# Kernel tuning notes

Measured on AMD Instinct MI355X. Metric: run time of the kernel, lower is better.

## Reference

```python
import jax, jax.numpy as jnp
import numpy as np

# Intersection(mode='product'):
#   a_fk = a @ feats.T            # [Na, K]
#   b_fk = b @ feats.T            # [Nb, K]
#   mask = (a_fk[:,None,:] > 0) & (b_fk[None,:,:] > 0)
#   result = sum_k (a_fk[:,None,:] * b_fk[None,:,:]) * mask   # [Na, Nb]
# For the product op, (x*y)*[x>0 & y>0] == relu(x)*relu(y) elementwise
# (any term with a non-positive factor is zeroed either way), so the
# broadcast+mask+reduce collapses exactly into a GEMM over relu'd scores.

def setup_inputs() -> dict:
    key = jax.random.key(0)
    k1, k2, k3 = jax.random.split(key, 3)
    a = jax.random.normal(k1, (1024, 2048), dtype=jnp.float32)
    b = jax.random.normal(k2, (1024, 2048), dtype=jnp.float32)
    feats = jax.random.normal(k3, (128, 2048), dtype=jnp.float32)
    return {"a": a, "b": b, "feats": feats}

def reference(a, b, feats):
    a_fk = a @ feats.T            # [Na, K]
    b_fk = b @ feats.T            # [Nb, K]
    # masked product-intersection reduced over K; identical math to the
    # broadcast (Na, Nb, K) -> sum formulation of the torch module.
    return jnp.einsum('ak,bk->ab', jax.nn.relu(a_fk), jax.nn.relu(b_fk))
```

## Files before the change

kernel.cpp:

```cpp
#include <hip/hip_runtime.h>


typedef __attribute__((ext_vector_type(8))) __bf16 bf16x8;
typedef __attribute__((ext_vector_type(4))) __bf16 bf16x4;
typedef __attribute__((ext_vector_type(4))) float floatx4;

#define KD     2048
#define NF     128
#define NA     1024
#define NPART  16
#define FKN    (2048 * 128)

static __device__ inline bf16x8 cvt8(float4 u, float4 v) {
    bf16x8 s;
    s[0] = (__bf16)u.x; s[1] = (__bf16)u.y; s[2] = (__bf16)u.z; s[3] = (__bf16)u.w;
    s[4] = (__bf16)v.x; s[5] = (__bf16)v.y; s[6] = (__bf16)v.z; s[7] = (__bf16)v.w;
    return s;
}

__global__ __launch_bounds__(256) void gemm1_part(const float* __restrict__ A,
                                                  const float* __restrict__ B,
                                                  const float* __restrict__ F,
                                                  float* __restrict__ part) {
    __shared__ __bf16 Xs[64 * 40];
    __shared__ __bf16 Fs[128 * 40];

    const int t    = threadIdx.x;
    const int m0   = blockIdx.x * 64;
    const int s    = blockIdx.y;
    const int k0   = s * 128;
    const float* src = (m0 < NA) ? (A + (size_t)m0 * KD)
                                 : (B + (size_t)(m0 - NA) * KD);

    const int lane = t & 63;
    const int w    = t >> 6;
    const int ln   = lane & 15;
    const int quad = lane >> 4;
    const int q8   = quad * 8;

    floatx4 acc[4][2];
#pragma unroll
    for (int mt = 0; mt < 4; mt++)
#pragma unroll
        for (int nt = 0; nt < 2; nt++)
            acc[mt][nt] = (floatx4){0.f, 0.f, 0.f, 0.f};

    const int xrow = t >> 2, xcol = (t & 3) * 8;
    const int frow = t >> 1, fcol = (t & 1) * 16;

#pragma unroll
    for (int kk = 0; kk < 128; kk += 32) {
        {
            const float* p = src + (size_t)xrow * KD + (k0 + kk + xcol);
            float4 u = *(const float4*)p;
            float4 v = *(const float4*)(p + 4);
            *(bf16x8*)&Xs[xrow * 40 + xcol] = cvt8(u, v);
        }
        {
            const float* p = F + (size_t)frow * KD + (k0 + kk + fcol);
            float4 u0 = *(const float4*)(p + 0);
            float4 u1 = *(const float4*)(p + 4);
            float4 u2 = *(const float4*)(p + 8);
            float4 u3 = *(const float4*)(p + 12);
            *(bf16x8*)&Fs[frow * 40 + fcol]     = cvt8(u0, u1);
            *(bf16x8*)&Fs[frow * 40 + fcol + 8] = cvt8(u2, u3);
        }
        __syncthreads();

        bf16x8 bfrag[2];
#pragma unroll
        for (int nt = 0; nt < 2; nt++)
            bfrag[nt] = *(const bf16x8*)&Fs[(w * 32 + nt * 16 + ln) * 40 + q8];
#pragma unroll
        for (int mt = 0; mt < 4; mt++) {
            bf16x8 af = *(const bf16x8*)&Xs[(mt * 16 + ln) * 40 + q8];
#pragma unroll
            for (int nt = 0; nt < 2; nt++)
                acc[mt][nt] = __builtin_amdgcn_mfma_f32_16x16x32_bf16(
                    af, bfrag[nt], acc[mt][nt], 0, 0, 0);
        }
        __syncthreads();
    }

    float* pdst = part + (size_t)s * FKN;
#pragma unroll
    for (int mt = 0; mt < 4; mt++)
#pragma unroll
        for (int nt = 0; nt < 2; nt++)
#pragma unroll
            for (int r = 0; r < 4; r++) {
                int row = m0 + mt * 16 + quad * 4 + r;
                int col = w * 32 + nt * 16 + ln;
                pdst[(size_t)row * NF + col] = acc[mt][nt][r];
            }
}

__global__ __launch_bounds__(256) void reduce_relu(const float* __restrict__ part,
                                                   __bf16* __restrict__ fkb) {
    int idx = blockIdx.x * 256 + threadIdx.x;
    size_t base = (size_t)idx * 4;
    float4 sum = make_float4(0.f, 0.f, 0.f, 0.f);
#pragma unroll
    for (int s = 0; s < NPART; s++) {
        float4 u = *(const float4*)(part + (size_t)s * FKN + base);
        sum.x += u.x; sum.y += u.y; sum.z += u.z; sum.w += u.w;
    }
    bf16x4 o;
    o[0] = (__bf16)fmaxf(sum.x, 0.f);
    o[1] = (__bf16)fmaxf(sum.y, 0.f);
    o[2] = (__bf16)fmaxf(sum.z, 0.f);
    o[3] = (__bf16)fmaxf(sum.w, 0.f);
    *(bf16x4*)(fkb + base) = o;
}

__global__ __launch_bounds__(256) void gemm2(const __bf16* __restrict__ fkb,
                                             float* __restrict__ out) {
    __shared__ __bf16 Ps[64 * 136];
    __shared__ __bf16 Qs[64 * 136];

    const int t    = threadIdx.x;
    const int i0   = blockIdx.y * 64;
    const int j0   = blockIdx.x * 64;
    const int lane = t & 63;
    const int w    = t >> 6;
    const int wm   = w & 1;
    const int wn   = w >> 1;
    const int ln   = lane & 15;
    const int quad = lane >> 4;
    const int q8   = quad * 8;

    const int prow = t >> 2, pcol = (t & 3) * 32;
    {
        const __bf16* p = fkb + (size_t)(i0 + prow) * NF + pcol;
        const __bf16* q = fkb + (size_t)(NA + j0 + prow) * NF + pcol;
#pragma unroll
        for (int c = 0; c < 32; c += 8) {
            *(bf16x8*)&Ps[prow * 136 + pcol + c] = *(const bf16x8*)(p + c);
            *(bf16x8*)&Qs[prow * 136 + pcol + c] = *(const bf16x8*)(q + c);
        }
    }
    __syncthreads();

    floatx4 acc[2][2];
#pragma unroll
    for (int mt = 0; mt < 2; mt++)
#pragma unroll
        for (int nt = 0; nt < 2; nt++)
            acc[mt][nt] = (floatx4){0.f, 0.f, 0.f, 0.f};

#pragma unroll
    for (int k0 = 0; k0 < 128; k0 += 32) {
        bf16x8 af[2], bf[2];
#pragma unroll
        for (int mt = 0; mt < 2; mt++)
            af[mt] = *(const bf16x8*)&Ps[(wm * 32 + mt * 16 + ln) * 136 + k0 + q8];
#pragma unroll
        for (int nt = 0; nt < 2; nt++)
            bf[nt] = *(const bf16x8*)&Qs[(wn * 32 + nt * 16 + ln) * 136 + k0 + q8];
#pragma unroll
        for (int mt = 0; mt < 2; mt++)
#pragma unroll
            for (int nt = 0; nt < 2; nt++)
                acc[mt][nt] = __builtin_amdgcn_mfma_f32_16x16x32_bf16(
                    af[mt], bf[nt], acc[mt][nt], 0, 0, 0);
    }

#pragma unroll
    for (int mt = 0; mt < 2; mt++)
#pragma unroll
        for (int nt = 0; nt < 2; nt++)
#pragma unroll
            for (int r = 0; r < 4; r++) {
                int row = i0 + wm * 32 + mt * 16 + quad * 4 + r;
                int col = j0 + wn * 32 + nt * 16 + ln;
                out[(size_t)row * 1024 + col] = acc[mt][nt][r];
            }
}

extern "C" void kernel_launch(void* const* d_in, const int* in_sizes, int n_in,
                              void* d_out, int out_size, void* d_ws, size_t ws_size,
                              hipStream_t stream) {
    const float* a     = (const float*)d_in[0];
    const float* b     = (const float*)d_in[1];
    const float* feats = (const float*)d_in[2];
    float* out = (float*)d_out;

    float*   part = (float*)d_ws;
    __bf16*  fkb  = (__bf16*)((char*)d_ws + (size_t)NPART * FKN * 4);

    gemm1_part<<<dim3(32, NPART), 256, 0, stream>>>(a, b, feats, part);
    reduce_relu<<<256, 256, 0, stream>>>(part, fkb);
    gemm2<<<dim3(16, 16), 256, 0, stream>>>(fkb, out);
}
```

Baseline: 80.19 us.

## Fuse three kernels into one cooperative kernel with grid syncs and register prefetch

Replaces the three launches (split-K GEMM, reduce+relu, second GEMM) with a single cooperative kernel of 512 blocks that uses grid-wide syncs between phases. It removes launch gaps and inter-kernel drain. It also prefetches the next K-slice into registers before the MFMA work in the first GEMM, and retiles the second GEMM to 64x32 tiles so the same 512 blocks cover the output. The cost is two grid barriers, a requirement that all 512 blocks be co-resident, and smaller per-block tiles in the second phase.

```diff
diff --git a/kernel.cpp b/kernel.cpp
--- a/kernel.cpp
+++ b/kernel.cpp
@@ -1,4 +1,7 @@
 #include <hip/hip_runtime.h>
+#include <hip/hip_cooperative_groups.h>
+
+namespace cg = cooperative_groups;
 
 
 typedef __attribute__((ext_vector_type(8))) __bf16 bf16x8;
@@ -18,163 +21,169 @@
     return s;
 }
 
-__global__ __launch_bounds__(256) void gemm1_part(const float* __restrict__ A,
-                                                  const float* __restrict__ B,
-                                                  const float* __restrict__ F,
-                                                  float* __restrict__ part) {
-    __shared__ __bf16 Xs[64 * 40];
-    __shared__ __bf16 Fs[128 * 40];
-
+__global__ __launch_bounds__(256, 2) void fused(const float* __restrict__ A,
+                                                const float* __restrict__ B,
+                                                const float* __restrict__ F,
+                                                float* __restrict__ part,
+                                                __bf16* __restrict__ fkb,
+                                                float* __restrict__ out) {
+    __shared__ __bf16 smem[64 * 136 + 32 * 136];
+
+    const int bid  = blockIdx.x;
     const int t    = threadIdx.x;
-    const int m0   = blockIdx.x * 64;
-    const int s    = blockIdx.y;
-    const int k0   = s * 128;
-    const float* src = (m0 < NA) ? (A + (size_t)m0 * KD)
-                                 : (B + (size_t)(m0 - NA) * KD);
-
     const int lane = t & 63;
     const int w    = t >> 6;
     const int ln   = lane & 15;
     const int quad = lane >> 4;
     const int q8   = quad * 8;
 
-    floatx4 acc[4][2];
-#pragma unroll
-    for (int mt = 0; mt < 4; mt++)
-#pragma unroll
-        for (int nt = 0; nt < 2; nt++)
-            acc[mt][nt] = (floatx4){0.f, 0.f, 0.f, 0.f};
-
-    const int xrow = t >> 2, xcol = (t & 3) * 8;
-    const int frow = t >> 1, fcol = (t & 1) * 16;
-
-#pragma unroll
-    for (int kk = 0; kk < 128; kk += 32) {
+    {
+        __bf16* Xs = smem;
+        __bf16* Fs = smem + 64 * 40;
+
+        const int bx = bid & 31;
+        const int s  = bid >> 5;
+        const int m0 = bx * 64;
+        const int k0 = s * 128;
+        const float* src = (m0 < NA) ? (A + (size_t)m0 * KD)
+                                     : (B + (size_t)(m0 - NA) * KD);
+
+        floatx4 acc[4][2];
+#pragma unroll
+        for (int mt = 0; mt < 4; mt++)
+#pragma unroll
+            for (int nt = 0; nt < 2; nt++)
+                acc[mt][nt] = (floatx4){0.f, 0.f, 0.f, 0.f};
+
+        const int xrow = t >> 2, xcol = (t & 3) * 8;
+        const int frow = t >> 1, fcol = (t & 1) * 16;
+        const float* xp = src + (size_t)xrow * KD + (k0 + xcol);
+        const float* fp = F   + (size_t)frow * KD + (k0 + fcol);
+
+        float4 xu = *(const float4*)(xp + 0);
+        float4 xv = *(const float4*)(xp + 4);
+        float4 f0 = *(const float4*)(fp + 0);
+        float4 f1 = *(const float4*)(fp + 4);
+        float4 f2 = *(const float4*)(fp + 8);
+        float4 f3 = *(const float4*)(fp + 12);
+
+#pragma unroll
+        for (int kk = 0; kk < 128; kk += 32) {
+            *(bf16x8*)&Xs[xrow * 40 + xcol]     = cvt8(xu, xv);
+            *(bf16x8*)&Fs[frow * 40 + fcol]     = cvt8(f0, f1);
+            *(bf16x8*)&Fs[frow * 40 + fcol + 8] = cvt8(f2, f3);
+            __syncthreads();
+
+            if (kk + 32 < 128) {
+                xu = *(const float4*)(xp + kk + 32);
+                xv = *(const float4*)(xp + kk + 36);
+                f0 = *(const float4*)(fp + kk + 32);
+                f1 = *(const float4*)(fp + kk + 36);
+                f2 = *(const float4*)(fp + kk + 40);
+                f3 = *(const float4*)(fp + kk + 44);
+            }
+
+            bf16x8 bfrag[2];
+#pragma unroll
+            for (int nt = 0; nt < 2; nt++)
+                bfrag[nt] = *(const bf16x8*)&Fs[(w * 32 + nt * 16 + ln) * 40 + q8];
+#pragma unroll
+            for (int mt = 0; mt < 4; mt++) {
+                bf16x8 af = *(const bf16x8*)&Xs[(mt * 16 + ln) * 40 + q8];
+#pragma unroll
+                for (int nt = 0; nt < 2; nt++)
+                    acc[mt][nt] = __builtin_amdgcn_mfma_f32_16x16x32_bf16(
+                        af, bfrag[nt], acc[mt][nt], 0, 0, 0);
+            }
+            __syncthreads();
+        }
+
+        float* pdst = part + (size_t)s * FKN;
+#pragma unroll
+        for (int mt = 0; mt < 4; mt++)
+#pragma unroll
+            for (int nt = 0; nt < 2; nt++)
+#pragma unroll
+                for (int r = 0; r < 4; r++) {
+                    int row = m0 + mt * 16 + quad * 4 + r;
+                    int col = w * 32 + nt * 16 + ln;
+                    pdst[(size_t)row * NF + col] = acc[mt][nt][r];
+                }
+    }
+
+    cg::this_grid().sync();
+
+    {
+        int idx = bid * 256 + t;
+        if (idx < 65536) {
+            size_t base = (size_t)idx * 4;
+            float4 sum = make_float4(0.f, 0.f, 0.f, 0.f);
+#pragma unroll
+            for (int s = 0; s < NPART; s++) {
+                float4 u = *(const float4*)(part + (size_t)s * FKN + base);
+                sum.x += u.x; sum.y += u.y; sum.z += u.z; sum.w += u.w;
+            }
+            bf16x4 o;
+            o[0] = (__bf16)fmaxf(sum.x, 0.f);
+            o[1] = (__bf16)fmaxf(sum.y, 0.f);
+            o[2] = (__bf16)fmaxf(sum.z, 0.f);
+            o[3] = (__bf16)fmaxf(sum.w, 0.f);
+            *(bf16x4*)(fkb + base) = o;
+        }
+    }
+
+    cg::this_grid().sync();
+
+    {
+        __bf16* Ps = smem;
+        __bf16* Qs = smem + 64 * 136;
+
+        const int i0 = (bid >> 5) * 64;
+        const int j0 = (bid & 31) * 32;
+
         {
-            const float* p = src + (size_t)xrow * KD + (k0 + kk + xcol);
-            float4 u = *(const float4*)p;
-            float4 v = *(const float4*)(p + 4);
-            *(bf16x8*)&Xs[xrow * 40 + xcol] = cvt8(u, v);
+            const int prow = t >> 2, pcol = (t & 3) * 32;
+            const __bf16* p = fkb + (size_t)(i0 + prow) * NF + pcol;
+#pragma unroll
+            for (int c = 0; c < 32; c += 8)
+                *(bf16x8*)&Ps[prow * 136 + pcol + c] = *(const bf16x8*)(p + c);
         }
         {
-            const float* p = F + (size_t)frow * KD + (k0 + kk + fcol);
-            float4 u0 = *(const float4*)(p + 0);
-            float4 u1 = *(const float4*)(p + 4);
-            float4 u2 = *(const float4*)(p + 8);
-            float4 u3 = *(const float4*)(p + 12);
-            *(bf16x8*)&Fs[frow * 40 + fcol]     = cvt8(u0, u1);
-            *(bf16x8*)&Fs[frow * 40 + fcol + 8] = cvt8(u2, u3);
+            const int qrow = t >> 3, qcol = (t & 7) * 16;
+            const __bf16* q = fkb + (size_t)(NA + j0 + qrow) * NF + qcol;
+#pragma unroll
+            for (int c = 0; c < 16; c += 8)
+                *(bf16x8*)&Qs[qrow * 136 + qcol + c] = *(const bf16x8*)(q + c);
         }
         __syncthreads();
 
-        bf16x8 bfrag[2];
-#pragma unroll
-        for (int nt = 0; nt < 2; nt++)
-            bfrag[nt] = *(const bf16x8*)&Fs[(w * 32 + nt * 16 + ln) * 40 + q8];
-#pragma unroll
-        for (int mt = 0; mt < 4; mt++) {
-            bf16x8 af = *(const bf16x8*)&Xs[(mt * 16 + ln) * 40 + q8];
-#pragma unroll
-            for (int nt = 0; nt < 2; nt++)
-                acc[mt][nt] = __builtin_amdgcn_mfma_f32_16x16x32_bf16(
-                    af, bfrag[nt], acc[mt][nt], 0, 0, 0);
-        }
-        __syncthreads();
-    }
-
-    float* pdst = part + (size_t)s * FKN;
-#pragma unroll
-    for (int mt = 0; mt < 4; mt++)
-#pragma unroll
-        for (int nt = 0; nt < 2; nt++)
-#pragma unroll
-            for (int r = 0; r < 4; r++) {
-                int row = m0 + mt * 16 + quad * 4 + r;
-                int col = w * 32 + nt * 16 + ln;
-                pdst[(size_t)row * NF + col] = acc[mt][nt][r];
-            }
-}
-
-__global__ __launch_bounds__(256) void reduce_relu(const float* __restrict__ part,
-                                                   __bf16* __restrict__ fkb) {
-    int idx = blockIdx.x * 256 + threadIdx.x;
-    size_t base = (size_t)idx * 4;
-    float4 sum = make_float4(0.f, 0.f, 0.f, 0.f);
-#pragma unroll
-    for (int s = 0; s < NPART; s++) {
-        float4 u = *(const float4*)(part + (size_t)s * FKN + base);
-        sum.x += u.x; sum.y += u.y; sum.z += u.z; sum.w += u.w;
-    }
-    bf16x4 o;
-    o[0] = (__bf16)fmaxf(sum.x, 0.f);
-    o[1] = (__bf16)fmaxf(sum.y, 0.f);
-    o[2] = (__bf16)fmaxf(sum.z, 0.f);
-    o[3] = (__bf16)fmaxf(sum.w, 0.f);
-    *(bf16x4*)(fkb + base) = o;
-}
-
-__global__ __launch_bounds__(256) void gemm2(const __bf16* __restrict__ fkb,
-                                             float* __restrict__ out) {
-    __shared__ __bf16 Ps[64 * 136];
-    __shared__ __bf16 Qs[64 * 136];
-
-    const int t    = threadIdx.x;
-    const int i0   = blockIdx.y * 64;
-    const int j0   = blockIdx.x * 64;
-    const int lane = t & 63;
-    const int w    = t >> 6;
-    const int wm   = w & 1;
-    const int wn   = w >> 1;
-    const int ln   = lane & 15;
-    const int quad = lane >> 4;
-    const int q8   = quad * 8;
-
-    const int prow = t >> 2, pcol = (t & 3) * 32;
-    {
-        const __bf16* p = fkb + (size_t)(i0 + prow) * NF + pcol;
-        const __bf16* q = fkb + (size_t)(NA + j0 + prow) * NF + pcol;
-#pragma unroll
-        for (int c = 0; c < 32; c += 8) {
-            *(bf16x8*)&Ps[prow * 136 + pcol + c] = *(const bf16x8*)(p + c);
-            *(bf16x8*)&Qs[prow * 136 + pcol + c] = *(const bf16x8*)(q + c);
-        }
-    }
-    __syncthreads();
-
-    floatx4 acc[2][2];
-#pragma unroll
-    for (int mt = 0; mt < 2; mt++)
-#pragma unroll
-        for (int nt = 0; nt < 2; nt++)
-            acc[mt][nt] = (floatx4){0.f, 0.f, 0.f, 0.f};
-
-#pragma unroll
-    for (int k0 = 0; k0 < 128; k0 += 32) {
-        bf16x8 af[2], bf[2];
+        const int wm = w & 1;
+        const int wn = w >> 1;
+
+        floatx4 acc2[2];
+        acc2[0] = (floatx4){0.f, 0.f, 0.f, 0.f};
+        acc2[1] = (floatx4){0.f, 0.f, 0.f, 0.f};
+
+#pragma unroll
+        for (int k0 = 0; k0 < 128; k0 += 32) {
+            bf16x8 bfq = *(const bf16x8*)&Qs[(wn * 16 + ln) * 136 + k0 + q8];
+#pragma unroll
+            for (int mt = 0; mt < 2; mt++) {
+                bf16x8 af = *(const bf16x8*)&Ps[(wm * 32 + mt * 16 + ln) * 136 + k0 + q8];
+                acc2[mt] = __builtin_amdgcn_mfma_f32_16x16x32_bf16(
+                    af, bfq, acc2[mt], 0, 0, 0);
+            }
+        }
+
 #pragma unroll
         for (int mt = 0; mt < 2; mt++)
-            af[mt] = *(const bf16x8*)&Ps[(wm * 32 + mt * 16 + ln) * 136 + k0 + q8];
-#pragma unroll
-        for (int nt = 0; nt < 2; nt++)
-            bf[nt] = *(const bf16x8*)&Qs[(wn * 32 + nt * 16 + ln) * 136 + k0 + q8];
-#pragma unroll
-        for (int mt = 0; mt < 2; mt++)
-#pragma unroll
-            for (int nt = 0; nt < 2; nt++)
-                acc[mt][nt] = __builtin_amdgcn_mfma_f32_16x16x32_bf16(
-                    af[mt], bf[nt], acc[mt][nt], 0, 0, 0);
-    }
-
-#pragma unroll
-    for (int mt = 0; mt < 2; mt++)
-#pragma unroll
-        for (int nt = 0; nt < 2; nt++)
 #pragma unroll
             for (int r = 0; r < 4; r++) {
                 int row = i0 + wm * 32 + mt * 16 + quad * 4 + r;
-                int col = j0 + wn * 32 + nt * 16 + ln;
-                out[(size_t)row * 1024 + col] = acc[mt][nt][r];
-            }
+                int col = j0 + wn * 16 + ln;
+                out[(size_t)row * 1024 + col] = acc2[mt][r];
+            }
+    }
 }
 
 extern "C" void kernel_launch(void* const* d_in, const int* in_sizes, int n_in,
@@ -188,7 +197,8 @@
     float*   part = (float*)d_ws;
     __bf16*  fkb  = (__bf16*)((char*)d_ws + (size_t)NPART * FKN * 4);
 
-    gemm1_part<<<dim3(32, NPART), 256, 0, stream>>>(a, b, feats, part);
-    reduce_relu<<<256, 256, 0, stream>>>(part, fkb);
-    gemm2<<<dim3(16, 16), 256, 0, stream>>>(fkb, out);
+    void* args[] = { (void*)&a, (void*)&b, (void*)&feats,
+                     (void*)&part, (void*)&fkb, (void*)&out };
+    hipLaunchCooperativeKernel((const void*)fused, dim3(512), dim3(256),
+                               args, 0, stream);
 }
```

Result: slower. 209.2 us (+160.9%).

## Halve split-K partitions, shrink row tile, prefetch next K chunk into registers

Applied to the files above, without the earlier changes.

The first GEMM now uses 8 split-K partitions of 256 columns each instead of 16 of 128, and a 32-row tile instead of 64, so the grid stays at 512 blocks. The partial-sum buffer and the reduce pass are halved. The next K chunk is loaded into registers while the MFMAs run on the current shared-memory tile, overlapping global loads with compute. The cost is that each F tile is reused across only 32 rows, so F is re-read from global memory more often.

```diff
diff --git a/kernel.cpp b/kernel.cpp
--- a/kernel.cpp
+++ b/kernel.cpp
@@ -8,7 +8,8 @@
 #define KD     2048
 #define NF     128
 #define NA     1024
-#define NPART  16
+#define NPART  8
+#define KSL    256
 #define FKN    (2048 * 128)
 
 static __device__ inline bf16x8 cvt8(float4 u, float4 v) {
@@ -18,17 +19,23 @@
     return s;
 }
 
-__global__ __launch_bounds__(256) void gemm1_part(const float* __restrict__ A,
-                                                  const float* __restrict__ B,
-                                                  const float* __restrict__ F,
-                                                  float* __restrict__ part) {
-    __shared__ __bf16 Xs[64 * 40];
+static __device__ inline bf16x4 cvt4(float4 u) {
+    bf16x4 s;
+    s[0] = (__bf16)u.x; s[1] = (__bf16)u.y; s[2] = (__bf16)u.z; s[3] = (__bf16)u.w;
+    return s;
+}
+
+__global__ __launch_bounds__(256) void gemm1_part8(const float* __restrict__ A,
+                                                   const float* __restrict__ B,
+                                                   const float* __restrict__ F,
+                                                   float* __restrict__ part) {
+    __shared__ __bf16 Xs[32 * 40];
     __shared__ __bf16 Fs[128 * 40];
 
     const int t    = threadIdx.x;
-    const int m0   = blockIdx.x * 64;
+    const int m0   = blockIdx.x * 32;
     const int s    = blockIdx.y;
-    const int k0   = s * 128;
+    const int k0   = s * KSL;
     const float* src = (m0 < NA) ? (A + (size_t)m0 * KD)
                                  : (B + (size_t)(m0 - NA) * KD);
 
@@ -38,41 +45,45 @@
     const int quad = lane >> 4;
     const int q8   = quad * 8;
 
-    floatx4 acc[4][2];
-#pragma unroll
-    for (int mt = 0; mt < 4; mt++)
+    floatx4 acc[2][2];
+#pragma unroll
+    for (int mt = 0; mt < 2; mt++)
 #pragma unroll
         for (int nt = 0; nt < 2; nt++)
             acc[mt][nt] = (floatx4){0.f, 0.f, 0.f, 0.f};
 
-    const int xrow = t >> 2, xcol = (t & 3) * 8;
+    const int xrow = t >> 3, xcol = (t & 7) * 4;
     const int frow = t >> 1, fcol = (t & 1) * 16;
-
-#pragma unroll
-    for (int kk = 0; kk < 128; kk += 32) {
-        {
-            const float* p = src + (size_t)xrow * KD + (k0 + kk + xcol);
-            float4 u = *(const float4*)p;
-            float4 v = *(const float4*)(p + 4);
-            *(bf16x8*)&Xs[xrow * 40 + xcol] = cvt8(u, v);
+    const float* xp = src + (size_t)xrow * KD + (k0 + xcol);
+    const float* fp = F   + (size_t)frow * KD + (k0 + fcol);
+
+    float4 xu = *(const float4*)(xp + 0);
+    float4 f0 = *(const float4*)(fp + 0);
+    float4 f1 = *(const float4*)(fp + 4);
+    float4 f2 = *(const float4*)(fp + 8);
+    float4 f3 = *(const float4*)(fp + 12);
+
+#pragma unroll
+    for (int kk = 0; kk < KSL; kk += 32) {
+        *(bf16x4*)&Xs[xrow * 40 + xcol]     = cvt4(xu);
+        *(bf16x8*)&Fs[frow * 40 + fcol]     = cvt8(f0, f1);
+        *(bf16x8*)&Fs[frow * 40 + fcol + 8] = cvt8(f2, f3);
+        __syncthreads();
+
+        if (kk + 32 < KSL) {
+            xu = *(const float4*)(xp + kk + 32);
+            f0 = *(const float4*)(fp + kk + 32);
+            f1 = *(const float4*)(fp + kk + 36);
+            f2 = *(const float4*)(fp + kk + 40);
+            f3 = *(const float4*)(fp + kk + 44);
         }
-        {
-            const float* p = F + (size_t)frow * KD + (k0 + kk + fcol);
-            float4 u0 = *(const float4*)(p + 0);
-            float4 u1 = *(const float4*)(p + 4);
-            float4 u2 = *(const float4*)(p + 8);
-            float4 u3 = *(const float4*)(p + 12);
-            *(bf16x8*)&Fs[frow * 40 + fcol]     = cvt8(u0, u1);
-            *(bf16x8*)&Fs[frow * 40 + fcol + 8] = cvt8(u2, u3);
-        }
-        __syncthreads();
 
         bf16x8 bfrag[2];
 #pragma unroll
         for (int nt = 0; nt < 2; nt++)
             bfrag[nt] = *(const bf16x8*)&Fs[(w * 32 + nt * 16 + ln) * 40 + q8];
 #pragma unroll
-        for (int mt = 0; mt < 4; mt++) {
+        for (int mt = 0; mt < 2; mt++) {
             bf16x8 af = *(const bf16x8*)&Xs[(mt * 16 + ln) * 40 + q8];
 #pragma unroll
             for (int nt = 0; nt < 2; nt++)
@@ -84,7 +95,7 @@
 
     float* pdst = part + (size_t)s * FKN;
 #pragma unroll
-    for (int mt = 0; mt < 4; mt++)
+    for (int mt = 0; mt < 2; mt++)
 #pragma unroll
         for (int nt = 0; nt < 2; nt++)
 #pragma unroll
@@ -188,7 +199,7 @@
     float*   part = (float*)d_ws;
     __bf16*  fkb  = (__bf16*)((char*)d_ws + (size_t)NPART * FKN * 4);
 
-    gemm1_part<<<dim3(32, NPART), 256, 0, stream>>>(a, b, feats, part);
+    gemm1_part8<<<dim3(64, NPART), 256, 0, stream>>>(a, b, feats, part);
     reduce_relu<<<256, 256, 0, stream>>>(part, fkb);
     gemm2<<<dim3(16, 16), 256, 0, stream>>>(fkb, out);
 }
```

After: 79.88 us. No clear change (-0.4%).
